# Performance work log

Measured on AMD Instinct MI355X. Metric: run time of the kernel, lower is better.

## Reference

```python
import math
import jax, jax.numpy as jnp
import numpy as np

D = 768
H = 12
P = 128  # sup_bdist
L = 512
B = 8
DH = D // H
EPS = 1e-5


def _ln(x, w, b):
    mu = jnp.mean(x, axis=-1, keepdims=True)
    var = jnp.mean(jnp.square(x - mu), axis=-1, keepdims=True)
    return (x - mu) * jax.lax.rsqrt(var + EPS) * w + b


def setup_inputs() -> dict:
    key = jax.random.key(0)
    ks = jax.random.split(key, 16)
    s_in = 1.0 / math.sqrt(D)
    s_ff = 1.0 / math.sqrt(4 * D)
    return {
        "x": jax.random.normal(ks[0], (L, B, D), jnp.float32),
        "edge": jax.random.normal(ks[1], (B * H, L, L), jnp.float32) * 0.1,
        "bdist": jax.random.randint(ks[2], (L, L, B), 0, P),
        "W_in": jax.random.uniform(ks[3], (3 * D, D), jnp.float32, -s_in, s_in),
        "b_in": jax.random.uniform(ks[4], (3 * D,), jnp.float32, -s_in, s_in),
        "pe_emb": jax.random.normal(ks[5], (P, D), jnp.float32),
        "W_out": jax.random.uniform(ks[6], (D, D), jnp.float32, -s_in, s_in),
        "b_out": jax.random.uniform(ks[7], (D,), jnp.float32, -s_in, s_in),
        "W1": jax.random.uniform(ks[8], (4 * D, D), jnp.float32, -s_in, s_in),
        "b1": jax.random.uniform(ks[9], (4 * D,), jnp.float32, -s_in, s_in),
        "W2": jax.random.uniform(ks[10], (D, 4 * D), jnp.float32, -s_ff, s_ff),
        "b2": jax.random.uniform(ks[11], (D,), jnp.float32, -s_ff, s_ff),
        "ln1_w": jnp.ones((D,), jnp.float32),
        "ln1_b": jnp.zeros((D,), jnp.float32),
        "ln2_w": jnp.ones((D,), jnp.float32),
        "ln2_b": jnp.zeros((D,), jnp.float32),
    }


def reference(x, edge, bdist, W_in, b_in, pe_emb, W_out, b_out,
              W1, b1, W2, b2, ln1_w, ln1_b, ln2_w, ln2_b):
    # x: [L,B,D], edge: [B*H,L,L], bdist: [L,L,B]
    x_res = x
    xn = _ln(x, ln1_w, ln1_b)
    qkv = xn @ W_in.T + b_in                      # [L,B,3D]
    q, k, v = jnp.split(qkv, 3, axis=-1)
    # -> [B,H,L,Dh]
    def to_bhld(t):
        return t.reshape(L, B, H, DH).transpose(1, 2, 0, 3)
    q, k, v = to_bhld(q), to_bhld(k), to_bhld(v)

    t = jnp.einsum('bhid,bhjd->bhij', q, k)      # QK^T

    # relative-position embeddings projected through the shared in_proj
    pe_proj = pe_emb @ W_in.T + b_in             # [P,3D]
    pe_q = pe_proj[:, :D].reshape(P, H, DH)
    pe_k = pe_proj[:, D:2 * D].reshape(P, H, DH)

    # pe_t_k[b,h,i,j] = <peq(bdist[i,j,b]), k[b,h,j]>;  pe_t_q analogous with q,pek
    kp = jnp.einsum('bhjd,phd->bhjp', k, pe_q)   # [B,H,L,P]
    qp = jnp.einsum('bhid,phd->bhip', q, pe_k)   # [B,H,L,P]
    idx = jnp.transpose(bdist, (2, 0, 1))        # [B,L,L]
    j_idx = jnp.arange(L)[None, :]               # broadcast over rows i
    i_idx = jnp.arange(L)[:, None]               # broadcast over cols j
    pe_t_k = jax.vmap(lambda kp_b, id_b: kp_b[:, j_idx, id_b])(kp, idx)  # [B,H,L,L]
    pe_t_q = jax.vmap(lambda qp_b, id_b: qp_b[:, i_idx, id_b])(qp, idx)  # [B,H,L,L]

    t = t + pe_t_k + pe_t_q
    dedge = t                                    # unscaled scores (no edge bias)
    inv = 1.0 / math.sqrt(DH)
    scores = t * inv + edge.reshape(B, H, L, L)
    attn = jax.nn.softmax(scores, axis=-1)
    o = jnp.einsum('bhij,bhjd->bhid', attn, v)   # [B,H,L,Dh]
    o = o.transpose(2, 0, 1, 3).reshape(L, B, D)
    o = o @ W_out.T + b_out

    x1 = x_res + o
    h = _ln(x1, ln2_w, ln2_b)
    ff = jax.nn.gelu(h @ W1.T + b1, approximate=False) @ W2.T + b2
    x_out = x1 + ff

    edge_out = edge + (dedge * inv).reshape(B * H, L, L)
    return x_out, edge_out
```

## Files before the change

### kernel.cpp

```cpp
#include <hip/hip_runtime.h>
#include <hip/hip_bf16.h>
#include <math.h>

#define LL 512
#define BB 8
#define DD 768
#define HH 12
#define DHH 64
#define PP 128

typedef unsigned char u8;
typedef unsigned short u16;
typedef unsigned int u32;
typedef __attribute__((ext_vector_type(8))) short bf16x8;
typedef __attribute__((ext_vector_type(4))) float f32x4;

__device__ __forceinline__ u16 f2bf(float f) {
  u32 u = __float_as_uint(f);
  u32 r = (u + 0x7fffu + ((u >> 16) & 1u)) >> 16;
  return (u16)r;
}
__device__ __forceinline__ float bf2f(u32 u) {
  return __uint_as_float((u & 0xffffu) << 16);
}

#define GLDS(g, l)                                                             \
  __builtin_amdgcn_global_load_lds(                                            \
      (const __attribute__((address_space(1))) void*)(g),                      \
      (__attribute__((address_space(3))) void*)(l), 16, 0, 0)

__device__ __forceinline__ void block_reduce2(float& a, float& b, float* sbuf) {
#pragma unroll
  for (int off = 32; off > 0; off >>= 1) {
    a += __shfl_down(a, off, 64);
    b += __shfl_down(b, off, 64);
  }
  int wid = threadIdx.x >> 6, lane = threadIdx.x & 63;
  __syncthreads();
  if (lane == 0) { sbuf[wid] = a; sbuf[4 + wid] = b; }
  __syncthreads();
  a = sbuf[0] + sbuf[1] + sbuf[2] + sbuf[3];
  b = sbuf[4] + sbuf[5] + sbuf[6] + sbuf[7];
}

__global__ __launch_bounds__(256) void ln_bf16(const float* __restrict__ x,
                                               const float* __restrict__ w,
                                               const float* __restrict__ bb,
                                               u16* __restrict__ out) {
  __shared__ float sbuf[8];
  size_t row = blockIdx.x;
  const float* xr = x + row * DD;
  int t = threadIdx.x;
  float v0 = xr[t], v1 = xr[t + 256], v2 = xr[t + 512];
  float s = v0 + v1 + v2;
  float ss = v0 * v0 + v1 * v1 + v2 * v2;
  block_reduce2(s, ss, sbuf);
  float mu = s * (1.0f / DD);
  float var = ss * (1.0f / DD) - mu * mu;
  float r = rsqrtf(var + 1e-5f);
  u16* orow = out + row * DD;
  orow[t]       = f2bf((v0 - mu) * r * w[t]       + bb[t]);
  orow[t + 256] = f2bf((v1 - mu) * r * w[t + 256] + bb[t + 256]);
  orow[t + 512] = f2bf((v2 - mu) * r * w[t + 512] + bb[t + 512]);
}

__global__ __launch_bounds__(256) void f2b_kernel(const float* __restrict__ in,
                                                  u16* __restrict__ out) {
  int idx = blockIdx.x * 256 + threadIdx.x;
  float4 v = *(const float4*)(in + (size_t)idx * 4);
  u32 lo = (u32)f2bf(v.x) | ((u32)f2bf(v.y) << 16);
  u32 hi = (u32)f2bf(v.z) | ((u32)f2bf(v.w) << 16);
  *(uint2*)(out + (size_t)idx * 4) = make_uint2(lo, hi);
}

__global__ __launch_bounds__(256) void f2b4_kernel(
    const float* __restrict__ i0, u16* __restrict__ o0,
    const float* __restrict__ i1, u16* __restrict__ o1,
    const float* __restrict__ i2, u16* __restrict__ o2,
    const float* __restrict__ i3, u16* __restrict__ o3) {
  int idx = blockIdx.x * 256 + threadIdx.x;
  const float* in;
  u16* out;
  if (idx < 442368) { in = i0; out = o0; }
  else if (idx < 589824) { in = i1; out = o1; idx -= 442368; }
  else if (idx < 1179648) { in = i2; out = o2; idx -= 589824; }
  else { in = i3; out = o3; idx -= 1179648; }
  float4 v = *(const float4*)(in + (size_t)idx * 4);
  u32 lo = (u32)f2bf(v.x) | ((u32)f2bf(v.y) << 16);
  u32 hi = (u32)f2bf(v.z) | ((u32)f2bf(v.w) << 16);
  *(uint2*)(out + (size_t)idx * 4) = make_uint2(lo, hi);
}

__global__ __launch_bounds__(256) void bdist_t(const int* __restrict__ bd,
                                               u8* __restrict__ out) {
  int t = blockIdx.x * 256 + threadIdx.x;
  int b = t & 7, jj = (t >> 3) & 511, ii = t >> 12;
  out[((size_t)b << 18) + ((size_t)ii << 9) + jj] = (u8)bd[t];
}

template <int ACT, int OBF, int RES>
__global__ __launch_bounds__(256) void gemm_mfma(
    const u16* __restrict__ A, int lda, const u16* __restrict__ B, int ldb,
    void* __restrict__ Cv, int ldc, const float* __restrict__ bias,
    const float* __restrict__ residual, int K) {
  __shared__ __align__(16) u16 Asl[128 * 32];
  __shared__ __align__(16) u16 Bsl[128 * 32];
  int t = threadIdx.x;
  int m0 = blockIdx.y * 128, n0 = blockIdx.x * 128;
  int lane = t & 63, w = t >> 6;
  int wr = w >> 1, wc = w & 1;
  int lr = lane & 15, lg = lane >> 4;

  f32x4 acc[4][4] = {};

  const u16* Ag0 = A + (size_t)(m0 + (t >> 2)) * lda + (t & 3) * 8;
  const u16* Ag1 = A + (size_t)(m0 + 64 + (t >> 2)) * lda + (t & 3) * 8;
  const u16* Bg0 = B + (size_t)(n0 + (t >> 2)) * ldb + (t & 3) * 8;
  const u16* Bg1 = B + (size_t)(n0 + 64 + (t >> 2)) * ldb + (t & 3) * 8;
  u16* Ad0 = &Asl[t * 8];
  u16* Ad1 = &Asl[2048 + t * 8];
  u16* Bd0 = &Bsl[t * 8];
  u16* Bd1 = &Bsl[2048 + t * 8];

  for (int k0 = 0; k0 < K; k0 += 32) {
    GLDS(Ag0 + k0, Ad0);
    GLDS(Ag1 + k0, Ad1);
    GLDS(Bg0 + k0, Bd0);
    GLDS(Bg1 + k0, Bd1);
    __syncthreads();
    bf16x8 a[4], b[4];
#pragma unroll
    for (int i = 0; i < 4; i++)
      a[i] = *(const bf16x8*)&Asl[(wr * 64 + i * 16 + lr) * 32 + lg * 8];
#pragma unroll
    for (int j = 0; j < 4; j++)
      b[j] = *(const bf16x8*)&Bsl[(wc * 64 + j * 16 + lr) * 32 + lg * 8];
#pragma unroll
    for (int i = 0; i < 4; i++)
#pragma unroll
      for (int j = 0; j < 4; j++)
        asm volatile("v_mfma_f32_16x16x32_bf16 %0, %1, %2, %0"
                     : "+v"(acc[i][j])
                     : "v"(a[i]), "v"(b[j]));
    __syncthreads();
  }
  asm volatile("s_nop 7\n\ts_nop 7" ::);

  float* Cf = (float*)Cv;
  u16* Cb = (u16*)Cv;
#pragma unroll
  for (int i = 0; i < 4; i++) {
#pragma unroll
    for (int r = 0; r < 4; r++) {
      int row = m0 + wr * 64 + i * 16 + lg * 4 + r;
#pragma unroll
      for (int j = 0; j < 4; j++) {
        int col = n0 + wc * 64 + j * 16 + lr;
        float vv = acc[i][j][r];
        if (bias) vv += bias[col];
        if (ACT) vv = 0.5f * vv * (1.0f + erff(vv * 0.70710678118654752f));
        if (RES) vv += residual[(size_t)row * ldc + col];
        if (OBF) Cb[(size_t)row * ldc + col] = f2bf(vv);
        else     Cf[(size_t)row * ldc + col] = vv;
      }
    }
  }
}

template <int BMOD>
__global__ __launch_bounds__(256) void gemm_mfma_b(
    const u16* __restrict__ A, int lda, long sAz,
    const u16* __restrict__ B, int ldb, long sBz,
    u16* __restrict__ Cb, int ldc, long sCz, int K) {
  __shared__ __align__(16) u16 Asl[128 * 32];
  __shared__ __align__(16) u16 Bsl[128 * 32];
  int z = blockIdx.z;
  A += (size_t)z * sAz;
  B += (size_t)(BMOD ? (z % HH) : z) * sBz;
  Cb += (size_t)z * sCz;
  int t = threadIdx.x;
  int m0 = blockIdx.y * 128, n0 = blockIdx.x * 128;
  int lane = t & 63, w = t >> 6;
  int wr = w >> 1, wc = w & 1;
  int lr = lane & 15, lg = lane >> 4;

  f32x4 acc[4][4] = {};

  const u16* Ag0 = A + (size_t)(m0 + (t >> 2)) * lda + (t & 3) * 8;
  const u16* Ag1 = A + (size_t)(m0 + 64 + (t >> 2)) * lda + (t & 3) * 8;
  const u16* Bg0 = B + (size_t)(n0 + (t >> 2)) * ldb + (t & 3) * 8;
  const u16* Bg1 = B + (size_t)(n0 + 64 + (t >> 2)) * ldb + (t & 3) * 8;
  u16* Ad0 = &Asl[t * 8];
  u16* Ad1 = &Asl[2048 + t * 8];
  u16* Bd0 = &Bsl[t * 8];
  u16* Bd1 = &Bsl[2048 + t * 8];

  for (int k0 = 0; k0 < K; k0 += 32) {
    GLDS(Ag0 + k0, Ad0);
    GLDS(Ag1 + k0, Ad1);
    GLDS(Bg0 + k0, Bd0);
    GLDS(Bg1 + k0, Bd1);
    __syncthreads();
    bf16x8 a[4], b[4];
#pragma unroll
    for (int i = 0; i < 4; i++)
      a[i] = *(const bf16x8*)&Asl[(wr * 64 + i * 16 + lr) * 32 + lg * 8];
#pragma unroll
    for (int j = 0; j < 4; j++)
      b[j] = *(const bf16x8*)&Bsl[(wc * 64 + j * 16 + lr) * 32 + lg * 8];
#pragma unroll
    for (int i = 0; i < 4; i++)
#pragma unroll
      for (int j = 0; j < 4; j++)
        asm volatile("v_mfma_f32_16x16x32_bf16 %0, %1, %2, %0"
                     : "+v"(acc[i][j])
                     : "v"(a[i]), "v"(b[j]));
    __syncthreads();
  }
  asm volatile("s_nop 7\n\ts_nop 7" ::);

#pragma unroll
  for (int i = 0; i < 4; i++) {
#pragma unroll
    for (int r = 0; r < 4; r++) {
      int row = m0 + wr * 64 + i * 16 + lg * 4 + r;
#pragma unroll
      for (int j = 0; j < 4; j++) {
        int col = n0 + wc * 64 + j * 16 + lr;
        Cb[(size_t)row * ldc + col] = f2bf(acc[i][j][r] * 0.125f);
      }
    }
  }
}

__global__ __launch_bounds__(256) void gemm_mfma_pe(
    const u16* __restrict__ kbp, const u16* __restrict__ qbp,
    const u16* __restrict__ peb, u16* __restrict__ kpb,
    u16* __restrict__ qpb) {
  __shared__ __align__(16) u16 Asl[128 * 32];
  __shared__ __align__(16) u16 Bsl[128 * 32];
  int z = blockIdx.z;
  int sel = z / 96, zz = z - sel * 96;
  const u16* A = (sel ? qbp : kbp) + (size_t)zz * (LL * DHH);
  const u16* B = peb + sel * DD + (size_t)(zz % HH) * 64;
  u16* Cb = (sel ? qpb : kpb) + (size_t)zz * (LL * PP);
  const int lda = DHH, ldb = 3 * DD, ldc = PP, K = DHH;
  int t = threadIdx.x;
  int m0 = blockIdx.y * 128, n0 = 0;
  int lane = t & 63, w = t >> 6;
  int wr = w >> 1, wc = w & 1;
  int lr = lane & 15, lg = lane >> 4;

  f32x4 acc[4][4] = {};

  const u16* Ag0 = A + (size_t)(m0 + (t >> 2)) * lda + (t & 3) * 8;
  const u16* Ag1 = A + (size_t)(m0 + 64 + (t >> 2)) * lda + (t & 3) * 8;
  const u16* Bg0 = B + (size_t)(n0 + (t >> 2)) * ldb + (t & 3) * 8;
  const u16* Bg1 = B + (size_t)(n0 + 64 + (t >> 2)) * ldb + (t & 3) * 8;
  u16* Ad0 = &Asl[t * 8];
  u16* Ad1 = &Asl[2048 + t * 8];
  u16* Bd0 = &Bsl[t * 8];
  u16* Bd1 = &Bsl[2048 + t * 8];

  for (int k0 = 0; k0 < K; k0 += 32) {
    GLDS(Ag0 + k0, Ad0);
    GLDS(Ag1 + k0, Ad1);
    GLDS(Bg0 + k0, Bd0);
    GLDS(Bg1 + k0, Bd1);
    __syncthreads();
    bf16x8 a[4], b[4];
#pragma unroll
    for (int i = 0; i < 4; i++)
      a[i] = *(const bf16x8*)&Asl[(wr * 64 + i * 16 + lr) * 32 + lg * 8];
#pragma unroll
    for (int j = 0; j < 4; j++)
      b[j] = *(const bf16x8*)&Bsl[(wc * 64 + j * 16 + lr) * 32 + lg * 8];
#pragma unroll
    for (int i = 0; i < 4; i++)
#pragma unroll
      for (int j = 0; j < 4; j++)
        asm volatile("v_mfma_f32_16x16x32_bf16 %0, %1, %2, %0"
                     : "+v"(acc[i][j])
                     : "v"(a[i]), "v"(b[j]));
    __syncthreads();
  }
  asm volatile("s_nop 7\n\ts_nop 7" ::);

#pragma unroll
  for (int i = 0; i < 4; i++) {
#pragma unroll
    for (int r = 0; r < 4; r++) {
      int row = m0 + wr * 64 + i * 16 + lg * 4 + r;
#pragma unroll
      for (int j = 0; j < 4; j++) {
        int col = n0 + wc * 64 + j * 16 + lr;
        Cb[(size_t)row * ldc + col] = f2bf(acc[i][j][r] * 0.125f);
      }
    }
  }
}

__global__ __launch_bounds__(256) void gemm_mfma_part(
    const u16* __restrict__ A, int lda, const u16* __restrict__ B, int ldb,
    float* __restrict__ Cf, int ldc, long partStride, int Kper) {
  __shared__ __align__(16) u16 Asl[128 * 32];
  __shared__ __align__(16) u16 Bsl[128 * 32];
  int z = blockIdx.z;
  A += (size_t)z * Kper;
  B += (size_t)z * Kper;
  Cf += (size_t)z * partStride;
  int t = threadIdx.x;
  int m0 = blockIdx.y * 128, n0 = blockIdx.x * 128;
  int lane = t & 63, w = t >> 6;
  int wr = w >> 1, wc = w & 1;
  int lr = lane & 15, lg = lane >> 4;

  f32x4 acc[4][4] = {};

  const u16* Ag0 = A + (size_t)(m0 + (t >> 2)) * lda + (t & 3) * 8;
  const u16* Ag1 = A + (size_t)(m0 + 64 + (t >> 2)) * lda + (t & 3) * 8;
  const u16* Bg0 = B + (size_t)(n0 + (t >> 2)) * ldb + (t & 3) * 8;
  const u16* Bg1 = B + (size_t)(n0 + 64 + (t >> 2)) * ldb + (t & 3) * 8;
  u16* Ad0 = &Asl[t * 8];
  u16* Ad1 = &Asl[2048 + t * 8];
  u16* Bd0 = &Bsl[t * 8];
  u16* Bd1 = &Bsl[2048 + t * 8];

  for (int k0 = 0; k0 < Kper; k0 += 32) {
    GLDS(Ag0 + k0, Ad0);
    GLDS(Ag1 + k0, Ad1);
    GLDS(Bg0 + k0, Bd0);
    GLDS(Bg1 + k0, Bd1);
    __syncthreads();
    bf16x8 a[4], b[4];
#pragma unroll
    for (int i = 0; i < 4; i++)
      a[i] = *(const bf16x8*)&Asl[(wr * 64 + i * 16 + lr) * 32 + lg * 8];
#pragma unroll
    for (int j = 0; j < 4; j++)
      b[j] = *(const bf16x8*)&Bsl[(wc * 64 + j * 16 + lr) * 32 + lg * 8];
#pragma unroll
    for (int i = 0; i < 4; i++)
#pragma unroll
      for (int j = 0; j < 4; j++)
        asm volatile("v_mfma_f32_16x16x32_bf16 %0, %1, %2, %0"
                     : "+v"(acc[i][j])
                     : "v"(a[i]), "v"(b[j]));
    __syncthreads();
  }
  asm volatile("s_nop 7\n\ts_nop 7" ::);

#pragma unroll
  for (int i = 0; i < 4; i++) {
#pragma unroll
    for (int r = 0; r < 4; r++) {
      int row = m0 + wr * 64 + i * 16 + lg * 4 + r;
#pragma unroll
      for (int j = 0; j < 4; j++) {
        int col = n0 + wc * 64 + j * 16 + lr;
        Cf[(size_t)row * ldc + col] = acc[i][j][r];
      }
    }
  }
}

template <int NS>
__global__ __launch_bounds__(256) void combine_k(const float* __restrict__ p,
                                                 const float* __restrict__ bias,
                                                 const float* __restrict__ res,
                                                 float* __restrict__ out) {
  int idx = blockIdx.x * 256 + threadIdx.x;
  size_t e = (size_t)idx * 4;
  float4 s = *(const float4*)(p + e);
#pragma unroll
  for (int z = 1; z < NS; z++) {
    float4 t2 = *(const float4*)(p + (size_t)z * 3145728 + e);
    s.x += t2.x; s.y += t2.y; s.z += t2.z; s.w += t2.w;
  }
  int col = (int)(e % DD);
  float4 b4 = *(const float4*)(bias + col);
  float4 r4 = *(const float4*)(res + e);
  *(float4*)(out + e) = make_float4(s.x + b4.x + r4.x, s.y + b4.y + r4.y,
                                    s.z + b4.z + r4.z, s.w + b4.w + r4.w);
}

__global__ __launch_bounds__(256) void combine2_ln(
    const float* __restrict__ p, const float* __restrict__ bias,
    const float* __restrict__ res, float* __restrict__ x1,
    const float* __restrict__ w, const float* __restrict__ lb,
    u16* __restrict__ xnb) {
  __shared__ float sbuf[8];
  size_t row = blockIdx.x;
  int t = threadIdx.x;
  const float* p0 = p + row * DD;
  const float* p1 = p + 3145728 + row * DD;
  const float* rr = res + row * DD;
  float v0 = p0[t]       + p1[t]       + bias[t]       + rr[t];
  float v1 = p0[t + 256] + p1[t + 256] + bias[t + 256] + rr[t + 256];
  float v2 = p0[t + 512] + p1[t + 512] + bias[t + 512] + rr[t + 512];
  float* xr = x1 + row * DD;
  xr[t] = v0; xr[t + 256] = v1; xr[t + 512] = v2;
  float s = v0 + v1 + v2;
  float ss = v0 * v0 + v1 * v1 + v2 * v2;
  block_reduce2(s, ss, sbuf);
  float mu = s * (1.0f / DD);
  float var = ss * (1.0f / DD) - mu * mu;
  float r = rsqrtf(var + 1e-5f);
  u16* orow = xnb + row * DD;
  orow[t]       = f2bf((v0 - mu) * r * w[t]       + lb[t]);
  orow[t + 256] = f2bf((v1 - mu) * r * w[t + 256] + lb[t + 256]);
  orow[t + 512] = f2bf((v2 - mu) * r * w[t + 512] + lb[t + 512]);
}

__global__ __launch_bounds__(256) void split_qkv6(const u16* __restrict__ qkvb,
                                                  u16* __restrict__ qb,
                                                  u16* __restrict__ kb,
                                                  u16* __restrict__ vbT) {
  int idx = blockIdx.x * 256 + threadIdx.x;
  int d4 = idx & 15;
  int l = (idx >> 4) & 511;
  int bh = idx >> 13;
  int b = bh / HH, h = bh - b * HH;
  size_t src = ((size_t)(l * BB + b)) * (3 * DD) + h * 64 + d4 * 4;
  uint2 qv = *(const uint2*)(qkvb + src);
  uint2 kv = *(const uint2*)(qkvb + src + DD);
  uint2 vv = *(const uint2*)(qkvb + src + 2 * DD);
  size_t dst = (size_t)idx * 4;
  *(uint2*)(qb + dst) = qv;
  *(uint2*)(kb + dst) = kv;
  u16 v0 = (u16)(vv.x & 0xffff), v1 = (u16)(vv.x >> 16);
  u16 v2 = (u16)(vv.y & 0xffff), v3 = (u16)(vv.y >> 16);
  size_t vtb = ((size_t)bh * DHH + d4 * 4) * LL + l;
  vbT[vtb]          = v0;
  vbT[vtb + LL]     = v1;
  vbT[vtb + 2 * LL] = v2;
  vbT[vtb + 3 * LL] = v3;
}

__global__ __launch_bounds__(256) void gather_scale2(
    const u16* __restrict__ tb,
    const u16* __restrict__ kp, const u16* __restrict__ qp,
    const u8* __restrict__ bdT, const float* __restrict__ edge,
    float* __restrict__ eout, float* __restrict__ stats) {
  int bh = blockIdx.z, b = bh / HH;
  int i0 = blockIdx.y * 64, j0 = blockIdx.x * 64, jt = blockIdx.x;
  __shared__ __align__(16) u16 kpl[64][PP];
  __shared__ __align__(16) u16 qpl[64][PP];
  int tid = threadIdx.x;
  int tx = tid & 15, ty = tid >> 4;

  const u16* kpg = kp + (size_t)bh * (LL * PP);
  const u16* qpg = qp + (size_t)bh * (LL * PP);
  u16* kflat = &kpl[0][0];
  u16* qflat = &qpl[0][0];
#pragma unroll
  for (int it = 0; it < 4; it++) {
    int c = tid + it * 256;
    int row = c >> 4, ch = (c & 15) * 8;
    GLDS(&kpg[(size_t)(j0 + row) * PP + ch], &kflat[c * 8]);
    GLDS(&qpg[(size_t)(i0 + row) * PP + ch], &qflat[c * 8]);
  }
  __syncthreads();

  const u8* bd = bdT + (size_t)b * (LL * LL);
  const float* eb = edge + (size_t)bh * (LL * LL);
  const u16* tbb = tb + (size_t)bh * (LL * LL);
  float* ob = eout + (size_t)bh * (LL * LL);

  float rowm[4], rows[4];
#pragma unroll
  for (int i2 = 0; i2 < 4; i2++) {
    int row = i0 + ty * 4 + i2;
    int col0 = j0 + tx * 4;
    uchar4 p4 = *(const uchar4*)&bd[(size_t)row * LL + col0];
    float4 e4 = *(const float4*)&eb[(size_t)row * LL + col0];
    uint2 t2 = *(const uint2*)&tbb[(size_t)row * LL + col0];
    float tv[4] = {bf2f(t2.x), bf2f(t2.x >> 16), bf2f(t2.y), bf2f(t2.y >> 16)};
    int pp[4] = {p4.x, p4.y, p4.z, p4.w};
    float ee[4] = {e4.x, e4.y, e4.z, e4.w};
    float sv[4];
#pragma unroll
    for (int j2 = 0; j2 < 4; j2++) {
      float gk = bf2f((u32)kpl[tx * 4 + j2][pp[j2]]);
      float gq = bf2f((u32)qpl[ty * 4 + i2][pp[j2]]);
      sv[j2] = tv[j2] + gk + gq + ee[j2];
    }
    *(float4*)&ob[(size_t)row * LL + col0] =
        make_float4(sv[0], sv[1], sv[2], sv[3]);
    float m = fmaxf(fmaxf(sv[0], sv[1]), fmaxf(sv[2], sv[3]));
#pragma unroll
    for (int off = 1; off < 16; off <<= 1) m = fmaxf(m, __shfl_xor(m, off, 64));
    float ss = expf(sv[0] - m) + expf(sv[1] - m) + expf(sv[2] - m) + expf(sv[3] - m);
#pragma unroll
    for (int off = 1; off < 16; off <<= 1) ss += __shfl_xor(ss, off, 64);
    rowm[i2] = m;
    rows[i2] = ss;
  }
  if (tx == 0) {
#pragma unroll
    for (int i2 = 0; i2 < 4; i2++) {
      size_t si = ((size_t)bh * LL + i0 + ty * 4 + i2) * 16 + jt;
      stats[si] = rowm[i2];
      stats[si + 8] = rows[i2];
    }
  }
}

__global__ __launch_bounds__(256) void softmax_pv_mfma(
    const float* __restrict__ scores, const u16* __restrict__ vbT,
    const float* __restrict__ stats, u16* __restrict__ olbd) {
  int bh = blockIdx.y;
  int i0 = blockIdx.x * 64;
  int b = bh / HH, h = bh - b * HH;
  __shared__ __align__(16) u16 PL[2][64 * 32];
  __shared__ __align__(16) u16 VL[2][64 * 32];
  __shared__ float smax[64], srs[64];
  int tid = threadIdx.x;
  int tx = tid & 15, ty = tid >> 4;
  int lane = tid & 63, w = tid >> 6;
  int wr = w >> 1, wc = w & 1;
  int lr = lane & 15, lg = lane >> 4;
  const float* sbase = scores + (size_t)bh * (LL * LL);
  const u16* vt = vbT + (size_t)bh * (DHH * LL);

  if (tid < 64) {
    size_t si = ((size_t)bh * LL + i0 + tid) * 16;
    float m = stats[si];
#pragma unroll
    for (int j = 1; j < 8; j++) m = fmaxf(m, stats[si + j]);
    float s = 0.f;
#pragma unroll
    for (int j = 0; j < 8; j++) s += stats[si + 8 + j] * expf(stats[si + j] - m);
    smax[tid] = m;
    srs[tid] = 1.0f / s;
  }
  __syncthreads();

  f32x4 acc[2][2] = {};
  int ks = tx >> 3, kk = (tx & 7) * 4;
  int vd = tid >> 2, vjo = (tid & 3) * 8;

  for (int jt = 0; jt < 8; jt++) {
    int j0 = jt * 64;
    GLDS(vt + (size_t)vd * LL + j0 + vjo, &VL[0][tid * 8]);
    GLDS(vt + (size_t)vd * LL + j0 + 32 + vjo, &VL[1][tid * 8]);
#pragma unroll
    for (int rr = 0; rr < 4; rr++) {
      int r = ty + rr * 16;
      float4 s4 = *(const float4*)(sbase + (size_t)(i0 + r) * LL + j0 + tx * 4);
      float m = smax[r], rs = srs[r];
      u16 p0 = f2bf(expf(s4.x - m) * rs);
      u16 p1 = f2bf(expf(s4.y - m) * rs);
      u16 p2 = f2bf(expf(s4.z - m) * rs);
      u16 p3 = f2bf(expf(s4.w - m) * rs);
      *(uint2*)&PL[ks][r * 32 + kk] =
          make_uint2((u32)p0 | ((u32)p1 << 16), (u32)p2 | ((u32)p3 << 16));
    }
    __syncthreads();
#pragma unroll
    for (int s2 = 0; s2 < 2; s2++) {
      bf16x8 a[2], bfr[2];
#pragma unroll
      for (int i = 0; i < 2; i++)
        a[i] = *(const bf16x8*)&PL[s2][(wr * 32 + i * 16 + lr) * 32 + lg * 8];
#pragma unroll
      for (int j = 0; j < 2; j++)
        bfr[j] = *(const bf16x8*)&VL[s2][(wc * 32 + j * 16 + lr) * 32 + lg * 8];
#pragma unroll
      for (int i = 0; i < 2; i++)
#pragma unroll
        for (int j = 0; j < 2; j++)
          asm volatile("v_mfma_f32_16x16x32_bf16 %0, %1, %2, %0"
                       : "+v"(acc[i][j])
                       : "v"(a[i]), "v"(bfr[j]));
    }
    __syncthreads();
  }
  asm volatile("s_nop 7\n\ts_nop 7" ::);

#pragma unroll
  for (int i = 0; i < 2; i++) {
#pragma unroll
    for (int r = 0; r < 4; r++) {
      int irow = i0 + wr * 32 + i * 16 + lg * 4 + r;
#pragma unroll
      for (int j = 0; j < 2; j++) {
        int d = wc * 32 + j * 16 + lr;
        olbd[((size_t)irow * BB + b) * DD + h * 64 + d] = f2bf(acc[i][j][r]);
      }
    }
  }
}

extern "C" void kernel_launch(void* const* d_in, const int* in_sizes, int n_in,
                              void* d_out, int out_size, void* d_ws, size_t ws_size,
                              hipStream_t stream) {
  const float* x      = (const float*)d_in[0];
  const float* edge   = (const float*)d_in[1];
  const int*   bdist  = (const int*)d_in[2];
  const float* W_in   = (const float*)d_in[3];
  const float* b_in   = (const float*)d_in[4];
  const float* pe_emb = (const float*)d_in[5];
  const float* W_out  = (const float*)d_in[6];
  const float* b_out  = (const float*)d_in[7];
  const float* W1     = (const float*)d_in[8];
  const float* b1     = (const float*)d_in[9];
  const float* W2     = (const float*)d_in[10];
  const float* b2     = (const float*)d_in[11];
  const float* ln1w   = (const float*)d_in[12];
  const float* ln1b   = (const float*)d_in[13];
  const float* ln2w   = (const float*)d_in[14];
  const float* ln2b   = (const float*)d_in[15];

  float* xout = (float*)d_out;
  float* eout = xout + (size_t)LL * BB * DD;

  float* ws = (float*)d_ws;
  u16*   xnb    = (u16*)(ws + 0);
  u16*   qkvb   = (u16*)(ws + 1600000);
  u16*   tb     = (u16*)(ws + 1600000);
  u16*   olbdb  = (u16*)(ws + 1600000);
  u16*   ff1b   = (u16*)(ws + 3200000);
  float* x1     = ws + 11100000;
  u16*   peemb  = (u16*)(ws + 14300000);
  float* part   = ws + 14600000;
  u16*   vbT    = (u16*)(ws + 21000000);
  float* stats  = ws + 22600000;
  u8*    bdT    = (u8*)(ws + 23400000);
  u16*   kpb    = (u16*)(ws + 24000000);
  u16*   qpb    = (u16*)(ws + 27200000);
  u16*   W1b    = (u16*)(ws + 30400000);
  u16*   W2b    = (u16*)(ws + 31600000);
  u16*   W_inb  = (u16*)(ws + 32800000);
  u16*   W_outb = (u16*)(ws + 33700000);
  u16*   qb     = (u16*)(ws + 34000000);
  u16*   kb     = (u16*)(ws + 35600000);
  u16*   peb    = (u16*)(ws + 37200000);

  f2b4_kernel<<<6912, 256, 0, stream>>>(W_in, W_inb, W_out, W_outb, W1, W1b,
                                        W2, W2b);
  f2b_kernel<<<96, 256, 0, stream>>>(pe_emb, peemb);
  bdist_t<<<8192, 256, 0, stream>>>(bdist, bdT);
  ln_bf16<<<4096, 256, 0, stream>>>(x, ln1w, ln1b, xnb);
  gemm_mfma<0, 1, 0><<<dim3(18, 32), 256, 0, stream>>>(
      xnb, DD, W_inb, DD, qkvb, 3 * DD, b_in, nullptr, DD);
  gemm_mfma<0, 1, 0><<<dim3(18, 1), 256, 0, stream>>>(
      peemb, DD, W_inb, DD, peb, 3 * DD, b_in, nullptr, DD);
  split_qkv6<<<3072, 256, 0, stream>>>(qkvb, qb, kb, vbT);
  gemm_mfma_pe<<<dim3(1, 4, 192), 256, 0, stream>>>(kb, qb, peb, kpb, qpb);
  gemm_mfma_b<0><<<dim3(4, 4, 96), 256, 0, stream>>>(
      qb, DHH, (long)LL * DHH, kb, DHH, (long)LL * DHH, tb, LL, (long)LL * LL,
      DHH);
  gather_scale2<<<dim3(8, 8, 96), 256, 0, stream>>>(tb, kpb, qpb, bdT, edge,
                                                    eout, stats);
  softmax_pv_mfma<<<dim3(8, 96), 256, 0, stream>>>(eout, vbT, stats, olbdb);
  gemm_mfma_part<<<dim3(6, 32, 2), 256, 0, stream>>>(
      olbdb, DD, W_outb, DD, part, DD, 3145728L, DD / 2);
  combine2_ln<<<4096, 256, 0, stream>>>(part, b_out, x, x1, ln2w, ln2b, xnb);
  gemm_mfma<1, 1, 0><<<dim3(24, 32), 256, 0, stream>>>(
      xnb, DD, W1b, DD, ff1b, 4 * DD, b1, nullptr, DD);
  gemm_mfma_part<<<dim3(6, 32, 4), 256, 0, stream>>>(
      ff1b, 4 * DD, W2b, 4 * DD, part, DD, 3145728L, DD);
  combine_k<4><<<3072, 256, 0, stream>>>(part, b2, x1, xout);
}
```

Baseline: 342.8 us.

## Merge prep kernels, fuse QKV split into GEMM epilogue, combine PE and QK GEMMs

```diff
diff --git a/kernel.cpp b/kernel.cpp
--- a/kernel.cpp
+++ b/kernel.cpp
@@ -43,59 +43,54 @@
   b = sbuf[4] + sbuf[5] + sbuf[6] + sbuf[7];
 }
 
-__global__ __launch_bounds__(256) void ln_bf16(const float* __restrict__ x,
-                                               const float* __restrict__ w,
-                                               const float* __restrict__ bb,
-                                               u16* __restrict__ out) {
-  __shared__ float sbuf[8];
-  size_t row = blockIdx.x;
-  const float* xr = x + row * DD;
+__global__ __launch_bounds__(256) void prep_kernel(
+    const float* __restrict__ x, const float* __restrict__ ln1w,
+    const float* __restrict__ ln1b, u16* __restrict__ xnb,
+    const float* __restrict__ W_in, u16* __restrict__ W_inb,
+    const float* __restrict__ W_out, u16* __restrict__ W_outb,
+    const float* __restrict__ W1, u16* __restrict__ W1b,
+    const float* __restrict__ W2, u16* __restrict__ W2b,
+    const float* __restrict__ pe_emb, u16* __restrict__ peemb,
+    const int* __restrict__ bdist, u8* __restrict__ bdT) {
+  int blk = blockIdx.x;
   int t = threadIdx.x;
-  float v0 = xr[t], v1 = xr[t + 256], v2 = xr[t + 512];
-  float s = v0 + v1 + v2;
-  float ss = v0 * v0 + v1 * v1 + v2 * v2;
-  block_reduce2(s, ss, sbuf);
-  float mu = s * (1.0f / DD);
-  float var = ss * (1.0f / DD) - mu * mu;
-  float r = rsqrtf(var + 1e-5f);
-  u16* orow = out + row * DD;
-  orow[t]       = f2bf((v0 - mu) * r * w[t]       + bb[t]);
-  orow[t + 256] = f2bf((v1 - mu) * r * w[t + 256] + bb[t + 256]);
-  orow[t + 512] = f2bf((v2 - mu) * r * w[t + 512] + bb[t + 512]);
-}
-
-__global__ __launch_bounds__(256) void f2b_kernel(const float* __restrict__ in,
-                                                  u16* __restrict__ out) {
-  int idx = blockIdx.x * 256 + threadIdx.x;
-  float4 v = *(const float4*)(in + (size_t)idx * 4);
-  u32 lo = (u32)f2bf(v.x) | ((u32)f2bf(v.y) << 16);
-  u32 hi = (u32)f2bf(v.z) | ((u32)f2bf(v.w) << 16);
-  *(uint2*)(out + (size_t)idx * 4) = make_uint2(lo, hi);
-}
-
-__global__ __launch_bounds__(256) void f2b4_kernel(
-    const float* __restrict__ i0, u16* __restrict__ o0,
-    const float* __restrict__ i1, u16* __restrict__ o1,
-    const float* __restrict__ i2, u16* __restrict__ o2,
-    const float* __restrict__ i3, u16* __restrict__ o3) {
-  int idx = blockIdx.x * 256 + threadIdx.x;
-  const float* in;
-  u16* out;
-  if (idx < 442368) { in = i0; out = o0; }
-  else if (idx < 589824) { in = i1; out = o1; idx -= 442368; }
-  else if (idx < 1179648) { in = i2; out = o2; idx -= 589824; }
-  else { in = i3; out = o3; idx -= 1179648; }
-  float4 v = *(const float4*)(in + (size_t)idx * 4);
-  u32 lo = (u32)f2bf(v.x) | ((u32)f2bf(v.y) << 16);
-  u32 hi = (u32)f2bf(v.z) | ((u32)f2bf(v.w) << 16);
-  *(uint2*)(out + (size_t)idx * 4) = make_uint2(lo, hi);
-}
-
-__global__ __launch_bounds__(256) void bdist_t(const int* __restrict__ bd,
-                                               u8* __restrict__ out) {
-  int t = blockIdx.x * 256 + threadIdx.x;
-  int b = t & 7, jj = (t >> 3) & 511, ii = t >> 12;
-  out[((size_t)b << 18) + ((size_t)ii << 9) + jj] = (u8)bd[t];
+  if (blk < 4096) {
+    __shared__ float sbuf[8];
+    const float* xr = x + (size_t)blk * DD;
+    float v0 = xr[t], v1 = xr[t + 256], v2 = xr[t + 512];
+    float s = v0 + v1 + v2;
+    float ss = v0 * v0 + v1 * v1 + v2 * v2;
+    block_reduce2(s, ss, sbuf);
+    float mu = s * (1.0f / DD);
+    float var = ss * (1.0f / DD) - mu * mu;
+    float r = rsqrtf(var + 1e-5f);
+    u16* orow = xnb + (size_t)blk * DD;
+    orow[t]       = f2bf((v0 - mu) * r * ln1w[t]       + ln1b[t]);
+    orow[t + 256] = f2bf((v1 - mu) * r * ln1w[t + 256] + ln1b[t + 256]);
+    orow[t + 512] = f2bf((v2 - mu) * r * ln1w[t + 512] + ln1b[t + 512]);
+  } else if (blk < 11008) {
+    int idx = (blk - 4096) * 256 + t;
+    const float* in;
+    u16* out;
+    if (idx < 442368) { in = W_in; out = W_inb; }
+    else if (idx < 589824) { in = W_out; out = W_outb; idx -= 442368; }
+    else if (idx < 1179648) { in = W1; out = W1b; idx -= 589824; }
+    else { in = W2; out = W2b; idx -= 1179648; }
+    float4 v = *(const float4*)(in + (size_t)idx * 4);
+    u32 lo = (u32)f2bf(v.x) | ((u32)f2bf(v.y) << 16);
+    u32 hi = (u32)f2bf(v.z) | ((u32)f2bf(v.w) << 16);
+    *(uint2*)(out + (size_t)idx * 4) = make_uint2(lo, hi);
+  } else if (blk < 11104) {
+    int idx = (blk - 11008) * 256 + t;
+    float4 v = *(const float4*)(pe_emb + (size_t)idx * 4);
+    u32 lo = (u32)f2bf(v.x) | ((u32)f2bf(v.y) << 16);
+    u32 hi = (u32)f2bf(v.z) | ((u32)f2bf(v.w) << 16);
+    *(uint2*)(peemb + (size_t)idx * 4) = make_uint2(lo, hi);
+  } else {
+    int i = (blk - 11104) * 256 + t;
+    int b = i & 7, jj = (i >> 3) & 511, ii = i >> 12;
+    bdT[((size_t)b << 18) + ((size_t)ii << 9) + jj] = (u8)bdist[i];
+  }
 }
 
 template <int ACT, int OBF, int RES>
@@ -167,17 +162,13 @@
   }
 }
 
-template <int BMOD>
-__global__ __launch_bounds__(256) void gemm_mfma_b(
-    const u16* __restrict__ A, int lda, long sAz,
-    const u16* __restrict__ B, int ldb, long sBz,
-    u16* __restrict__ Cb, int ldc, long sCz, int K) {
+__global__ __launch_bounds__(256) void gemm_mfma_qkv(
+    const u16* __restrict__ A, const u16* __restrict__ B,
+    const float* __restrict__ bias, u16* __restrict__ qb,
+    u16* __restrict__ kb, u16* __restrict__ vtmp) {
   __shared__ __align__(16) u16 Asl[128 * 32];
   __shared__ __align__(16) u16 Bsl[128 * 32];
-  int z = blockIdx.z;
-  A += (size_t)z * sAz;
-  B += (size_t)(BMOD ? (z % HH) : z) * sBz;
-  Cb += (size_t)z * sCz;
+  const int lda = DD, ldb = DD, K = DD;
   int t = threadIdx.x;
   int m0 = blockIdx.y * 128, n0 = blockIdx.x * 128;
   int lane = t & 63, w = t >> 6;
@@ -224,29 +215,70 @@
 #pragma unroll
     for (int r = 0; r < 4; r++) {
       int row = m0 + wr * 64 + i * 16 + lg * 4 + r;
+      int l = row >> 3, b = row & 7;
 #pragma unroll
       for (int j = 0; j < 4; j++) {
         int col = n0 + wc * 64 + j * 16 + lr;
-        Cb[(size_t)row * ldc + col] = f2bf(acc[i][j][r] * 0.125f);
+        u16 vv = f2bf(acc[i][j][r] + bias[col]);
+        int which = col / DD, hd = col - which * DD;
+        if (which == 0) {
+          int h = hd >> 6, d = hd & 63;
+          qb[(((size_t)(b * HH + h)) * LL + l) * DHH + d] = vv;
+        } else if (which == 1) {
+          int h = hd >> 6, d = hd & 63;
+          kb[(((size_t)(b * HH + h)) * LL + l) * DHH + d] = vv;
+        } else {
+          vtmp[(size_t)row * DD + hd] = vv;
+        }
       }
     }
   }
 }
 
-__global__ __launch_bounds__(256) void gemm_mfma_pe(
-    const u16* __restrict__ kbp, const u16* __restrict__ qbp,
+__global__ __launch_bounds__(256) void split_v(const u16* __restrict__ vtmp,
+                                               u16* __restrict__ vbT) {
+  int idx = blockIdx.x * 256 + threadIdx.x;
+  int d4 = idx & 15;
+  int l = (idx >> 4) & 511;
+  int bh = idx >> 13;
+  int b = bh / HH, h = bh - b * HH;
+  size_t src = ((size_t)(l * BB + b)) * DD + h * 64 + d4 * 4;
+  uint2 vv = *(const uint2*)(vtmp + src);
+  u16 v0 = (u16)(vv.x & 0xffff), v1 = (u16)(vv.x >> 16);
+  u16 v2 = (u16)(vv.y & 0xffff), v3 = (u16)(vv.y >> 16);
+  size_t vtb = ((size_t)bh * DHH + d4 * 4) * LL + l;
+  vbT[vtb]          = v0;
+  vbT[vtb + LL]     = v1;
+  vbT[vtb + 2 * LL] = v2;
+  vbT[vtb + 3 * LL] = v3;
+}
+
+__global__ __launch_bounds__(256) void attn_k64(
+    const u16* __restrict__ qb, const u16* __restrict__ kb,
     const u16* __restrict__ peb, u16* __restrict__ kpb,
-    u16* __restrict__ qpb) {
+    u16* __restrict__ qpb, u16* __restrict__ tb) {
   __shared__ __align__(16) u16 Asl[128 * 32];
   __shared__ __align__(16) u16 Bsl[128 * 32];
-  int z = blockIdx.z;
-  int sel = z / 96, zz = z - sel * 96;
-  const u16* A = (sel ? qbp : kbp) + (size_t)zz * (LL * DHH);
-  const u16* B = peb + sel * DD + (size_t)(zz % HH) * 64;
-  u16* Cb = (sel ? qpb : kpb) + (size_t)zz * (LL * PP);
-  const int lda = DHH, ldb = 3 * DD, ldc = PP, K = DHH;
+  int id = blockIdx.x;
+  const u16 *A, *B;
+  u16* Cb;
+  int lda, ldb, ldc, m0, n0;
+  if (id < 768) {
+    int my = id & 3, z = id >> 2;
+    int sel = z / 96, zz = z - sel * 96;
+    A = (sel ? qb : kb) + (size_t)zz * (LL * DHH);
+    B = peb + sel * DD + (size_t)(zz % HH) * 64;
+    Cb = (sel ? qpb : kpb) + (size_t)zz * (LL * PP);
+    lda = DHH; ldb = 3 * DD; ldc = PP; m0 = my * 128; n0 = 0;
+  } else {
+    int id2 = id - 768;
+    int jx = id2 & 3, my = (id2 >> 2) & 3, bh = id2 >> 4;
+    A = qb + (size_t)bh * (LL * DHH);
+    B = kb + (size_t)bh * (LL * DHH);
+    Cb = tb + (size_t)bh * (LL * LL);
+    lda = DHH; ldb = DHH; ldc = LL; m0 = my * 128; n0 = jx * 128;
+  }
   int t = threadIdx.x;
-  int m0 = blockIdx.y * 128, n0 = 0;
   int lane = t & 63, w = t >> 6;
   int wr = w >> 1, wc = w & 1;
   int lr = lane & 15, lg = lane >> 4;
@@ -262,7 +294,7 @@
   u16* Bd0 = &Bsl[t * 8];
   u16* Bd1 = &Bsl[2048 + t * 8];
 
-  for (int k0 = 0; k0 < K; k0 += 32) {
+  for (int k0 = 0; k0 < DHH; k0 += 32) {
     GLDS(Ag0 + k0, Ad0);
     GLDS(Ag1 + k0, Ad1);
     GLDS(Bg0 + k0, Bd0);
@@ -412,31 +444,6 @@
   orow[t + 512] = f2bf((v2 - mu) * r * w[t + 512] + lb[t + 512]);
 }
 
-__global__ __launch_bounds__(256) void split_qkv6(const u16* __restrict__ qkvb,
-                                                  u16* __restrict__ qb,
-                                                  u16* __restrict__ kb,
-                                                  u16* __restrict__ vbT) {
-  int idx = blockIdx.x * 256 + threadIdx.x;
-  int d4 = idx & 15;
-  int l = (idx >> 4) & 511;
-  int bh = idx >> 13;
-  int b = bh / HH, h = bh - b * HH;
-  size_t src = ((size_t)(l * BB + b)) * (3 * DD) + h * 64 + d4 * 4;
-  uint2 qv = *(const uint2*)(qkvb + src);
-  uint2 kv = *(const uint2*)(qkvb + src + DD);
-  uint2 vv = *(const uint2*)(qkvb + src + 2 * DD);
-  size_t dst = (size_t)idx * 4;
-  *(uint2*)(qb + dst) = qv;
-  *(uint2*)(kb + dst) = kv;
-  u16 v0 = (u16)(vv.x & 0xffff), v1 = (u16)(vv.x >> 16);
-  u16 v2 = (u16)(vv.y & 0xffff), v3 = (u16)(vv.y >> 16);
-  size_t vtb = ((size_t)bh * DHH + d4 * 4) * LL + l;
-  vbT[vtb]          = v0;
-  vbT[vtb + LL]     = v1;
-  vbT[vtb + 2 * LL] = v2;
-  vbT[vtb + 3 * LL] = v3;
-}
-
 __global__ __launch_bounds__(256) void gather_scale2(
     const u16* __restrict__ tb,
     const u16* __restrict__ kp, const u16* __restrict__ qp,
@@ -617,12 +624,12 @@
 
   float* ws = (float*)d_ws;
   u16*   xnb    = (u16*)(ws + 0);
-  u16*   qkvb   = (u16*)(ws + 1600000);
   u16*   tb     = (u16*)(ws + 1600000);
   u16*   olbdb  = (u16*)(ws + 1600000);
   u16*   ff1b   = (u16*)(ws + 3200000);
   float* x1     = ws + 11100000;
   u16*   peemb  = (u16*)(ws + 14300000);
+  u16*   vtmp   = (u16*)(ws + 14600000);
   float* part   = ws + 14600000;
   u16*   vbT    = (u16*)(ws + 21000000);
   float* stats  = ws + 22600000;
@@ -637,20 +644,15 @@
   u16*   kb     = (u16*)(ws + 35600000);
   u16*   peb    = (u16*)(ws + 37200000);
 
-  f2b4_kernel<<<6912, 256, 0, stream>>>(W_in, W_inb, W_out, W_outb, W1, W1b,
-                                        W2, W2b);
-  f2b_kernel<<<96, 256, 0, stream>>>(pe_emb, peemb);
-  bdist_t<<<8192, 256, 0, stream>>>(bdist, bdT);
-  ln_bf16<<<4096, 256, 0, stream>>>(x, ln1w, ln1b, xnb);
-  gemm_mfma<0, 1, 0><<<dim3(18, 32), 256, 0, stream>>>(
-      xnb, DD, W_inb, DD, qkvb, 3 * DD, b_in, nullptr, DD);
+  prep_kernel<<<19296, 256, 0, stream>>>(x, ln1w, ln1b, xnb, W_in, W_inb,
+                                         W_out, W_outb, W1, W1b, W2, W2b,
+                                         pe_emb, peemb, bdist, bdT);
+  gemm_mfma_qkv<<<dim3(18, 32), 256, 0, stream>>>(xnb, W_inb, b_in, qb, kb,
+                                                  vtmp);
   gemm_mfma<0, 1, 0><<<dim3(18, 1), 256, 0, stream>>>(
       peemb, DD, W_inb, DD, peb, 3 * DD, b_in, nullptr, DD);
-  split_qkv6<<<3072, 256, 0, stream>>>(qkvb, qb, kb, vbT);
-  gemm_mfma_pe<<<dim3(1, 4, 192), 256, 0, stream>>>(kb, qb, peb, kpb, qpb);
-  gemm_mfma_b<0><<<dim3(4, 4, 96), 256, 0, stream>>>(
-      qb, DHH, (long)LL * DHH, kb, DHH, (long)LL * DHH, tb, LL, (long)LL * LL,
-      DHH);
+  split_v<<<3072, 256, 0, stream>>>(vtmp, vbT);
+  attn_k64<<<2304, 256, 0, stream>>>(qb, kb, peb, kpb, qpb, tb);
   gather_scale2<<<dim3(8, 8, 96), 256, 0, stream>>>(tb, kpb, qpb, bdT, edge,
                                                     eout, stats);
   softmax_pv_mfma<<<dim3(8, 96), 256, 0, stream>>>(eout, vbT, stats, olbdb);
```

New measurement: 328.8 us. 1.04x faster.
